# Optimization experiments

Hardware: AMD Instinct MI355X
Metric: run time of the kernel (lower is better)

The kernel has to match this reference:

```python
import jax, jax.numpy as jnp
import numpy as np

D_MODEL = 1024
N_HEADS = 16
HEAD_DIM = D_MODEL // N_HEADS


def setup_inputs() -> dict:
    key = jax.random.key(0)
    k1, k2, k3 = jax.random.split(key, 3)
    x = jax.random.normal(k1, (4, 2048, D_MODEL), dtype=jnp.float32)
    # torch nn.Linear(d_model, 3*d_model, bias=False): weight [3C, C], y = x @ W.T
    w_qkv = jax.random.normal(k2, (3 * D_MODEL, D_MODEL), dtype=jnp.float32) * (1.0 / np.sqrt(D_MODEL))
    w_out = jax.random.normal(k3, (D_MODEL, D_MODEL), dtype=jnp.float32) * (1.0 / np.sqrt(D_MODEL))
    return {"x": x, "w_qkv": w_qkv, "w_out": w_out}


def reference(x, w_qkv, w_out):
    B, T, C = x.shape
    H, Dh = N_HEADS, HEAD_DIM
    scale = 1.0 / np.sqrt(Dh).astype(np.float32)
    qkv = x @ w_qkv.T  # [B, T, 3C]
    q, k, v = jnp.split(qkv, 3, axis=-1)

    def heads(t):  # [B,T,C] -> [B,H,T,Dh]
        return t.reshape(B, T, H, Dh).transpose(0, 2, 1, 3)

    q, k, v = heads(q), heads(k), heads(v)
    attn = jnp.einsum('bhqd,bhkd->bhqk', q, k) * scale  # [B,H,T,T]
    attn = jax.nn.softmax(attn, axis=-1)
    out = jnp.einsum('bhqk,bhkd->bhqd', attn, v)  # [B,H,T,Dh]
    out = out.transpose(0, 2, 1, 3).reshape(B, T, C)
    return out @ w_out.T
```

## Files before the change

kernel.cpp:

```cpp
#include <hip/hip_runtime.h>
#include <hip/hip_bf16.h>

#define DEVINL __device__ __forceinline__

typedef short s16x8 __attribute__((ext_vector_type(8)));
typedef float f32x4 __attribute__((ext_vector_type(4)));

static constexpr int TC = 1024;
static constexpr int NH = 16;
static constexpr int DH = 64;
static constexpr int TT = 2048;
static constexpr int NB = 4;
static constexpr int MROWS = NB * TT;

static constexpr float QSCALE = 0.18033688011112042f;

DEVINL ushort f32_to_bf16u(float f) {
  uint u = __builtin_bit_cast(uint, f);
  u += 0x7fffu + ((u >> 16) & 1u);
  return (ushort)(u >> 16);
}

DEVINL f32x4 mfma32(s16x8 a, s16x8 b, f32x4 c) {
  return __builtin_amdgcn_mfma_f32_16x16x32_bf16(a, b, c, 0, 0, 0);
}

DEVINL void gload_lds16(const void* g, void* l) {
  __builtin_amdgcn_global_load_lds((const __attribute__((address_space(1))) void*)g,
                                   (__attribute__((address_space(3))) void*)l, 16, 0, 0);
}

DEVINL s16x8 ld8(const ushort* p) { return *reinterpret_cast<const s16x8*>(p); }

DEVINL void cvt_range(const float* __restrict__ src, ushort* __restrict__ dst, int n4,
                      int i0, int stride) {
  for (int i = i0; i < n4; i += stride) {
    float4 v = reinterpret_cast<const float4*>(src)[i];
    ushort4 o;
    o.x = f32_to_bf16u(v.x);
    o.y = f32_to_bf16u(v.y);
    o.z = f32_to_bf16u(v.z);
    o.w = f32_to_bf16u(v.w);
    reinterpret_cast<ushort4*>(dst)[i] = o;
  }
}

__global__ void cvt3_kernel(const float* __restrict__ s0, ushort* __restrict__ d0, int n0,
                            const float* __restrict__ s1, ushort* __restrict__ d1, int n1,
                            const float* __restrict__ s2, ushort* __restrict__ d2, int n2) {
  const int i0 = blockIdx.x * blockDim.x + threadIdx.x;
  const int stride = gridDim.x * blockDim.x;
  cvt_range(s0, d0, n0, i0, stride);
  cvt_range(s1, d1, n1, i0, stride);
  cvt_range(s2, d2, n2, i0, stride);
}

template <int MODE>
__global__ __launch_bounds__(256, 2) void gemm_bt(
    const ushort* __restrict__ A, const ushort* __restrict__ Bw, float* __restrict__ Cout,
    ushort* __restrict__ Qo, ushort* __restrict__ Ko, ushort* __restrict__ Vo, int N) {
  __shared__ __align__(16) ushort As[2][128 * 64];
  __shared__ __align__(16) ushort Bs[2][128 * 64];
  const int tid = threadIdx.x;
  const int lane = tid & 63;
  const int wid = tid >> 6;
  const int bx = blockIdx.x, by = blockIdx.y;
  const int wrow = (wid >> 1) * 64, wcol = (wid & 1) * 64;
  const int lr = lane >> 3;
  const int lc = lane & 7;

  f32x4 acc[4][4] = {};

#define GSTAGE(buf, kt)                                                         \
  {                                                                             \
    _Pragma("unroll") for (int j = 0; j < 4; ++j) {                             \
      const int seg = wid * 4 + j;                                              \
      const int r = seg * 8 + lr;                                               \
      const int csrc = lc ^ (r & 7);                                            \
      gload_lds16(A + (size_t)(by * 128 + r) * TC + (kt) + csrc * 8,            \
                  &As[buf][seg * 512]);                                         \
      gload_lds16(Bw + (size_t)(bx * 128 + r) * TC + (kt) + csrc * 8,           \
                  &Bs[buf][seg * 512]);                                         \
    }                                                                           \
  }

  GSTAGE(0, 0);
  __syncthreads();

  for (int t = 0; t < TC / 64; ++t) {
    const int buf = t & 1;
    if (t + 1 < TC / 64) GSTAGE(buf ^ 1, (t + 1) * 64);
#pragma unroll
    for (int kk = 0; kk < 2; ++kk) {
      s16x8 af[4], bfr[4];
#pragma unroll
      for (int m = 0; m < 4; ++m) {
        const int r = wrow + m * 16 + (lane & 15);
        const int ch = (kk * 4 + (lane >> 4)) ^ (r & 7);
        af[m] = ld8(&As[buf][r * 64 + ch * 8]);
      }
#pragma unroll
      for (int n = 0; n < 4; ++n) {
        const int r = wcol + n * 16 + (lane & 15);
        const int ch = (kk * 4 + (lane >> 4)) ^ (r & 7);
        bfr[n] = ld8(&Bs[buf][r * 64 + ch * 8]);
      }
#pragma unroll
      for (int m = 0; m < 4; ++m)
#pragma unroll
        for (int n = 0; n < 4; ++n) acc[m][n] = mfma32(af[m], bfr[n], acc[m][n]);
    }
    __syncthreads();
  }
#undef GSTAGE

#pragma unroll
  for (int m = 0; m < 4; ++m) {
#pragma unroll
    for (int n = 0; n < 4; ++n) {
      const int ng = bx * 128 + wcol + n * 16 + (lane & 15);
      const int mg0 = by * 128 + wrow + m * 16 + (lane >> 4) * 4;
      if (MODE == 0) {
#pragma unroll
        for (int i = 0; i < 4; ++i) Cout[(size_t)(mg0 + i) * N + ng] = acc[m][n][i];
      } else {
        const int sec = ng >> 10;
        const int w = ng & 1023;
        const int h = w >> 6, d = w & 63;
        const int t0 = mg0 & (TT - 1);
        const int b = mg0 >> 11;
        const int bh = b * NH + h;
        if (sec == 0) {
#pragma unroll
          for (int i = 0; i < 4; ++i)
            Qo[((size_t)bh * TT + t0 + i) * DH + d] = f32_to_bf16u(acc[m][n][i] * QSCALE);
        } else if (sec == 1) {
#pragma unroll
          for (int i = 0; i < 4; ++i)
            Ko[((size_t)bh * TT + t0 + i) * DH + d] = f32_to_bf16u(acc[m][n][i]);
        } else {
          ushort4 o;
          o.x = f32_to_bf16u(acc[m][n][0]);
          o.y = f32_to_bf16u(acc[m][n][1]);
          o.z = f32_to_bf16u(acc[m][n][2]);
          o.w = f32_to_bf16u(acc[m][n][3]);
          *reinterpret_cast<ushort4*>(&Vo[((size_t)bh * DH + d) * TT + t0]) = o;
        }
      }
    }
  }
}

__global__ __launch_bounds__(256, 4) void attn_kernel(const ushort* __restrict__ Q,
                                                      const ushort* __restrict__ K,
                                                      const ushort* __restrict__ V,
                                                      ushort* __restrict__ O) {
  __shared__ __align__(16) ushort Ks[2][64 * 64];
  __shared__ __align__(16) ushort Vs[2][64 * 64];
  const int tid = threadIdx.x;
  const int lane = tid & 63, wid = tid >> 6;
  const int bh = blockIdx.x;
  const int q0 = blockIdx.y * 128 + wid * 32;
  const int qr = lane & 15, lg = lane >> 4;

  const ushort* Qh = Q + (size_t)bh * TT * DH;
  const ushort* Kh = K + (size_t)bh * TT * DH;
  const ushort* Vh = V + (size_t)bh * DH * TT;

  s16x8 qf[2][2];
#pragma unroll
  for (int qt = 0; qt < 2; ++qt)
#pragma unroll
    for (int h = 0; h < 2; ++h)
      qf[qt][h] = ld8(&Qh[(q0 + qt * 16 + qr) * DH + h * 32 + lg * 8]);

  const int pk = 8 * (qr >> 2) + (qr & 3);

  const uint one_bf = 0x3F803F80u;
  const s16x8 ONES = __builtin_bit_cast(s16x8, (uint4){one_bf, one_bf, one_bf, one_bf});

  f32x4 acc[2][4] = {};
  f32x4 acc1[2] = {};

#define SWZ(r) ((r ^ ((r & 8) >> 1)) & 7)

  int koff[2][2][2], voff[2][4];
#pragma unroll
  for (int kh = 0; kh < 2; ++kh) {
#pragma unroll
    for (int jj = 0; jj < 2; ++jj)
#pragma unroll
      for (int h = 0; h < 2; ++h) {
        const int r = kh * 32 + pk + 4 * jj;
        koff[kh][jj][h] = r * 64 + ((h * 4 + lg) ^ SWZ(r)) * 8;
      }
#pragma unroll
    for (int g = 0; g < 4; ++g) {
      const int r = g * 16 + qr;
      voff[kh][g] = r * 64 + ((kh * 4 + lg) ^ SWZ(r)) * 8;
    }
  }

#define STAGE(buf, k0)                                                              \
  {                                                                                 \
    _Pragma("unroll") for (int j = 0; j < 2; ++j) {                                 \
      const int l = tid + 256 * j;                                                  \
      const int row = l >> 3, ch = l & 7;                                           \
      const int sc = ch ^ SWZ(row);                                                 \
      gload_lds16(&Kh[(size_t)((k0) + row) * DH + sc * 8],                          \
                  &Ks[buf][(wid * 64 + 256 * j) * 8]);                              \
      gload_lds16(&Vh[(size_t)row * TT + (k0) + sc * 8],                            \
                  &Vs[buf][(wid * 64 + 256 * j) * 8]);                              \
    }                                                                               \
  }

  STAGE(0, 0);
  __syncthreads();

  for (int t = 0; t < TT / 64; ++t) {
    const int buf = t & 1;
    if (t + 1 < TT / 64) STAGE(buf ^ 1, (t + 1) * 64);
    const ushort* Kb = Ks[buf];
    const ushort* Vb = Vs[buf];

#pragma unroll
    for (int kh = 0; kh < 2; ++kh) {
      s16x8 kf[2][2];
#pragma unroll
      for (int jj = 0; jj < 2; ++jj)
#pragma unroll
        for (int h = 0; h < 2; ++h) kf[jj][h] = ld8(&Kb[koff[kh][jj][h]]);
      s16x8 vf[4];
#pragma unroll
      for (int g = 0; g < 4; ++g) vf[g] = ld8(&Vb[voff[kh][g]]);

#pragma unroll
      for (int qt = 0; qt < 2; ++qt) {
        const f32x4 z = {};
        __builtin_amdgcn_s_setprio(1);
        f32x4 slo = mfma32(kf[0][0], qf[qt][0], z);
        slo = mfma32(kf[0][1], qf[qt][1], slo);
        f32x4 shi = mfma32(kf[1][0], qf[qt][0], z);
        shi = mfma32(kf[1][1], qf[qt][1], shi);
        __builtin_amdgcn_s_setprio(0);

        float p[8];
#pragma unroll
        for (int i = 0; i < 4; ++i) {
          p[i] = __builtin_amdgcn_exp2f(slo[i]);
          p[4 + i] = __builtin_amdgcn_exp2f(shi[i]);
        }

        uint u[4];
#pragma unroll
        for (int e = 0; e < 4; ++e)
          asm("v_cvt_pk_bf16_f32 %0, %1, %2" : "=v"(u[e]) : "v"(p[2 * e]), "v"(p[2 * e + 1]));
        const s16x8 pa = __builtin_bit_cast(s16x8, u);

        __builtin_amdgcn_s_setprio(1);
#pragma unroll
        for (int g = 0; g < 4; ++g) acc[qt][g] = mfma32(pa, vf[g], acc[qt][g]);
        acc1[qt] = mfma32(pa, ONES, acc1[qt]);
        __builtin_amdgcn_s_setprio(0);
      }
    }
    __syncthreads();
  }

  const int b = bh >> 4, h = bh & 15;
#pragma unroll
  for (int qt = 0; qt < 2; ++qt) {
    float inv[4];
#pragma unroll
    for (int i = 0; i < 4; ++i) inv[i] = 1.0f / acc1[qt][i];
#pragma unroll
    for (int g = 0; g < 4; ++g) {
#pragma unroll
      for (int i = 0; i < 4; ++i) {
        const int tq = q0 + qt * 16 + lg * 4 + i;
        const int col = h * DH + g * 16 + qr;
        O[((size_t)b * TT + tq) * TC + col] = f32_to_bf16u(acc[qt][g][i] * inv[i]);
      }
    }
  }
#undef STAGE
#undef SWZ
}

extern "C" void kernel_launch(void* const* d_in, const int* in_sizes, int n_in,
                              void* d_out, int out_size, void* d_ws, size_t ws_size,
                              hipStream_t stream) {
  const float* x = (const float*)d_in[0];
  const float* wqkv = (const float*)d_in[1];
  const float* wout = (const float*)d_in[2];
  float* out = (float*)d_out;
  char* ws = (char*)d_ws;

  ushort* xb    = (ushort*)(ws);
  ushort* wqkvb = (ushort*)(ws + ((size_t)16 << 20));
  ushort* woutb = (ushort*)(ws + ((size_t)22 << 20));
  ushort* qb    = (ushort*)(ws + ((size_t)24 << 20));
  ushort* kb    = (ushort*)(ws + ((size_t)40 << 20));
  ushort* vtb   = (ushort*)(ws + ((size_t)56 << 20));

  cvt3_kernel<<<2048, 256, 0, stream>>>(x, xb, MROWS * TC / 4,
                                        wqkv, wqkvb, 3 * TC * TC / 4,
                                        wout, woutb, TC * TC / 4);

  gemm_bt<1><<<dim3(3 * TC / 128, MROWS / 128), 256, 0, stream>>>(
      xb, wqkvb, nullptr, qb, kb, vtb, 3 * TC);

  attn_kernel<<<dim3(NB * NH, TT / 128), 256, 0, stream>>>(qb, kb, vtb, xb);

  gemm_bt<0><<<dim3(TC / 128, MROWS / 128), 256, 0, stream>>>(
      xb, woutb, out, nullptr, nullptr, nullptr, TC);
}
```

Measured before the change: 175.3 us.

## Enlarge GEMM tiles to 256x128 with 512 threads and triple-buffered LDS pipeline

The QKV and output-projection GEMMs now use 512-thread blocks computing 256x128 tiles. Each B tile is shared across twice as many rows, which halves the global B traffic per output. The LDS staging goes from double to triple buffering, with explicit vmcnt waits and raw s_barrier calls so loads run two stages ahead instead of a full __syncthreads each iteration. LDS use rises to about 144KB per block, so occupancy is likely limited to a single block per CU despite the launch bound of 2. The hand-counted vmcnt values must match the issued loads exactly.

```diff
diff --git a/kernel.cpp b/kernel.cpp
--- a/kernel.cpp
+++ b/kernel.cpp
@@ -56,40 +56,55 @@
 }
 
 template <int MODE>
-__global__ __launch_bounds__(256, 2) void gemm_bt(
+__global__ __launch_bounds__(512, 2) void gemm_bt(
     const ushort* __restrict__ A, const ushort* __restrict__ Bw, float* __restrict__ Cout,
     ushort* __restrict__ Qo, ushort* __restrict__ Ko, ushort* __restrict__ Vo, int N) {
-  __shared__ __align__(16) ushort As[2][128 * 64];
-  __shared__ __align__(16) ushort Bs[2][128 * 64];
+  __shared__ __align__(16) ushort As[3][256 * 64];
+  __shared__ __align__(16) ushort Bs[3][128 * 64];
   const int tid = threadIdx.x;
   const int lane = tid & 63;
   const int wid = tid >> 6;
   const int bx = blockIdx.x, by = blockIdx.y;
-  const int wrow = (wid >> 1) * 64, wcol = (wid & 1) * 64;
-  const int lr = lane >> 3;
-  const int lc = lane & 7;
+  const int wrow = (wid >> 1) * 64;
+  const int wcol = (wid & 1) * 64;
 
   f32x4 acc[4][4] = {};
 
-#define GSTAGE(buf, kt)                                                         \
+#define GSTAGE(slot, kt)                                                        \
   {                                                                             \
     _Pragma("unroll") for (int j = 0; j < 4; ++j) {                             \
-      const int seg = wid * 4 + j;                                              \
-      const int r = seg * 8 + lr;                                               \
-      const int csrc = lc ^ (r & 7);                                            \
-      gload_lds16(A + (size_t)(by * 128 + r) * TC + (kt) + csrc * 8,            \
-                  &As[buf][seg * 512]);                                         \
-      gload_lds16(Bw + (size_t)(bx * 128 + r) * TC + (kt) + csrc * 8,           \
-                  &Bs[buf][seg * 512]);                                         \
+      const int flat = j * 512 + tid;                                           \
+      const int r = flat >> 3, ch = flat & 7;                                   \
+      const int sc = ch ^ (r & 7);                                              \
+      gload_lds16(A + (size_t)(by * 256 + r) * TC + (kt) + sc * 8,              \
+                  &As[slot][flat * 8]);                                         \
     }                                                                           \
+    _Pragma("unroll") for (int j = 0; j < 2; ++j) {                             \
+      const int flat = j * 512 + tid;                                           \
+      const int r = flat >> 3, ch = flat & 7;                                   \
+      const int sc = ch ^ (r & 7);                                              \
+      gload_lds16(Bw + (size_t)(bx * 128 + r) * TC + (kt) + sc * 8,             \
+                  &Bs[slot][flat * 8]);                                         \
+    }                                                                           \
   }
 
   GSTAGE(0, 0);
-  __syncthreads();
-
-  for (int t = 0; t < TC / 64; ++t) {
-    const int buf = t & 1;
-    if (t + 1 < TC / 64) GSTAGE(buf ^ 1, (t + 1) * 64);
+  GSTAGE(1, 64);
+
+  for (int t = 0; t < 16; ++t) {
+    if (t <= 13) GSTAGE((t + 2) % 3, (t + 2) * 64);
+    if (t <= 13)
+      asm volatile("s_waitcnt vmcnt(12)" ::: "memory");
+    else if (t == 14)
+      asm volatile("s_waitcnt vmcnt(6)" ::: "memory");
+    else
+      asm volatile("s_waitcnt vmcnt(0)" ::: "memory");
+    __builtin_amdgcn_sched_barrier(0);
+    __builtin_amdgcn_s_barrier();
+    __builtin_amdgcn_sched_barrier(0);
+
+    const ushort* Ab = As[t % 3];
+    const ushort* Bb = Bs[t % 3];
 #pragma unroll
     for (int kk = 0; kk < 2; ++kk) {
       s16x8 af[4], bfr[4];
@@ -97,20 +112,21 @@
       for (int m = 0; m < 4; ++m) {
         const int r = wrow + m * 16 + (lane & 15);
         const int ch = (kk * 4 + (lane >> 4)) ^ (r & 7);
-        af[m] = ld8(&As[buf][r * 64 + ch * 8]);
+        af[m] = ld8(&Ab[r * 64 + ch * 8]);
       }
 #pragma unroll
       for (int n = 0; n < 4; ++n) {
         const int r = wcol + n * 16 + (lane & 15);
         const int ch = (kk * 4 + (lane >> 4)) ^ (r & 7);
-        bfr[n] = ld8(&Bs[buf][r * 64 + ch * 8]);
+        bfr[n] = ld8(&Bb[r * 64 + ch * 8]);
       }
 #pragma unroll
       for (int m = 0; m < 4; ++m)
 #pragma unroll
         for (int n = 0; n < 4; ++n) acc[m][n] = mfma32(af[m], bfr[n], acc[m][n]);
     }
-    __syncthreads();
+    __builtin_amdgcn_sched_barrier(0);
+    __builtin_amdgcn_s_barrier();
   }
 #undef GSTAGE
 
@@ -119,7 +135,7 @@
 #pragma unroll
     for (int n = 0; n < 4; ++n) {
       const int ng = bx * 128 + wcol + n * 16 + (lane & 15);
-      const int mg0 = by * 128 + wrow + m * 16 + (lane >> 4) * 4;
+      const int mg0 = by * 256 + wrow + m * 16 + (lane >> 4) * 4;
       if (MODE == 0) {
 #pragma unroll
         for (int i = 0; i < 4; ++i) Cout[(size_t)(mg0 + i) * N + ng] = acc[m][n][i];
@@ -307,11 +323,11 @@
                                         wqkv, wqkvb, 3 * TC * TC / 4,
                                         wout, woutb, TC * TC / 4);
 
-  gemm_bt<1><<<dim3(3 * TC / 128, MROWS / 128), 256, 0, stream>>>(
+  gemm_bt<1><<<dim3(3 * TC / 128, MROWS / 256), 512, 0, stream>>>(
       xb, wqkvb, nullptr, qb, kb, vtb, 3 * TC);
 
   attn_kernel<<<dim3(NB * NH, TT / 128), 256, 0, stream>>>(qb, kb, vtb, xb);
 
-  gemm_bt<0><<<dim3(TC / 128, MROWS / 128), 256, 0, stream>>>(
+  gemm_bt<0><<<dim3(TC / 128, MROWS / 256), 512, 0, stream>>>(
       xb, woutb, out, nullptr, nullptr, nullptr, TC);
 }
```

Result: slower. 191.2 us (+9.1%).
